# Kernel tuning notes

Hardware: AMD Instinct MI355X
Metric: run time of the kernel (lower is better)

The kernel has to match this reference:

```python
import jax, jax.numpy as jnp
import numpy as np

N, D, B = 8192, 512, 64
EPS = 1e-5


def _layernorm(x, w, b):
    mu = jnp.mean(x, axis=-1, keepdims=True)
    var = jnp.mean(jnp.square(x - mu), axis=-1, keepdims=True)
    return (x - mu) * jax.lax.rsqrt(var + EPS) * w + b


def setup_inputs() -> dict:
    key = jax.random.key(0)
    ks = jax.random.split(key, 10)
    s = 0.02
    return {
        "x_mole": jax.random.normal(ks[0], (N, D), jnp.float32),
        "x_conf": jax.random.normal(ks[1], (N, D), jnp.float32),
        "W1": jax.random.normal(ks[2], (D, D), jnp.float32) * s,   # attention_1 (no bias)
        "W2": jax.random.normal(ks[3], (D, D), jnp.float32) * s,   # attention_2 (no bias)
        "phi1_w": jnp.ones((D,), jnp.float32),
        "phi1_b": jnp.zeros((D,), jnp.float32),
        "phi2_w": jnp.ones((D,), jnp.float32),
        "phi2_b": jnp.zeros((D,), jnp.float32),
        "rho_w1": jax.random.normal(ks[4], (D, D), jnp.float32) * s,
        "rho_b1": jnp.zeros((D,), jnp.float32),
        "rho_w2": jax.random.normal(ks[5], (D, D), jnp.float32) * s,
        "rho_b2": jnp.zeros((D,), jnp.float32),
        "rho_ln_w": jnp.ones((D,), jnp.float32),
        "rho_ln_b": jnp.zeros((D,), jnp.float32),
        "batch": jnp.sort(jax.random.randint(ks[6], (N,), 0, B, jnp.int64)),
    }


def reference(x_mole, x_conf, W1, W2, phi1_w, phi1_b, phi2_w, phi2_b,
              rho_w1, rho_b1, rho_w2, rho_b2, rho_ln_w, rho_ln_b, batch):
    # projections of LayerNormed inputs (torch Linear: y = x @ W^T)
    q = _layernorm(x_mole, phi1_w, phi1_b) @ W1.T          # [N, D]
    k = _layernorm(x_conf, phi2_w, phi2_b) @ W2.T          # [N, D]
    dot = q @ k.T                                          # [N, N]

    # block-diagonal batch-equality mask and hand-rolled masked softmax
    mask = (batch[:, None] == batch[None, :]).astype(dot.dtype)  # [N, N]
    max_values = jnp.max(dot * mask, axis=1, keepdims=True)
    masked = (dot - max_values) * mask
    e = jnp.exp(masked)
    attn = e / jnp.sum(e * mask, axis=1, keepdims=True)
    attn = attn * mask                                     # [N, N]

    x_weighted = attn @ x_conf                             # [N, D]

    # rho MLP: Linear -> SiLU -> Linear -> SiLU -> LayerNorm
    h = jax.nn.silu(x_weighted @ rho_w1.T + rho_b1)
    h = jax.nn.silu(h @ rho_w2.T + rho_b2)
    x_encoded = _layernorm(h, rho_ln_w, rho_ln_b)
    return x_encoded, attn
```

## Files before the change

kernel.cpp:

```cpp
#include <hip/hip_runtime.h>

namespace {

constexpr int N = 8192;
constexpr int D = 512;
constexpr int NBATCH = 64;
constexpr int SEGMAX = 256;
constexpr int XCW = NBATCH * SEGMAX;
constexpr size_t MB = 1u << 20;

using s16x8 = __attribute__((ext_vector_type(8))) short;
using f32x4 = __attribute__((ext_vector_type(4))) float;

__device__ inline short f2bf(float f) {
  unsigned u = __float_as_uint(f);
  u += 0x7fffu + ((u >> 16) & 1u);
  return (short)(u >> 16);
}
__device__ inline float bf2f(short h) {
  return __uint_as_float(((unsigned)(unsigned short)h) << 16);
}
__device__ inline void split2(float f, short& hi, short& lo) {
  hi = f2bf(f);
  lo = f2bf(f - bf2f(hi));
}

__device__ inline f32x4 mfma16(s16x8 a, s16x8 b, f32x4 c) {
  return __builtin_amdgcn_mfma_f32_16x16x32_bf16(a, b, c, 0, 0, 0);
}

__device__ inline void gl16(const short* g, short* l) {
  __builtin_amdgcn_global_load_lds((const __attribute__((address_space(1))) void*)g,
                                   (__attribute__((address_space(3))) void*)l, 16, 0, 0);
}

template <int Nn>
__device__ inline void vmw() {
  asm volatile("s_waitcnt vmcnt(%0)" ::"i"(Nn) : "memory");
}

__device__ inline void ln_row(const float* __restrict__ x, const float* __restrict__ w,
                              const float* __restrict__ bsrc, int row, int lane,
                              float o[8]) {
  const float* xr = x + (size_t)row * D + lane * 8;
  f32x4 v0 = *(const f32x4*)xr;
  f32x4 v1 = *(const f32x4*)(xr + 4);
  float s = 0.f, sq = 0.f;
#pragma unroll
  for (int j = 0; j < 4; j++) {
    s += v0[j] + v1[j];
    sq += v0[j] * v0[j] + v1[j] * v1[j];
  }
#pragma unroll
  for (int off = 32; off >= 1; off >>= 1) {
    s += __shfl_xor(s, off);
    sq += __shfl_xor(sq, off);
  }
  float mu = s * (1.f / D);
  float var = sq * (1.f / D) - mu * mu;
  float rs = rsqrtf(var + 1e-5f);
  const float* wp = w + lane * 8;
  const float* bp = bsrc + lane * 8;
  f32x4 w0 = *(const f32x4*)wp, w1 = *(const f32x4*)(wp + 4);
  f32x4 b0 = *(const f32x4*)bp, b1 = *(const f32x4*)(bp + 4);
#pragma unroll
  for (int j = 0; j < 4; j++) {
    o[j] = (v0[j] - mu) * rs * w0[j] + b0[j];
    o[j + 4] = (v1[j] - mu) * rs * w1[j] + b1[j];
  }
}

__global__ __launch_bounds__(256) void prep_kernel(
    const float* __restrict__ x_mole, const float* __restrict__ phi1_w,
    const float* __restrict__ phi1_b, short* __restrict__ xm_hi, short* __restrict__ xm_lo,
    const float* __restrict__ x_conf, const float* __restrict__ phi2_w,
    const float* __restrict__ phi2_b, short* __restrict__ xc_hi, short* __restrict__ xc_lo,
    const float* __restrict__ W1, const float* __restrict__ W2,
    const float* __restrict__ rho_w1, const float* __restrict__ rho_w2,
    short* __restrict__ w1h, short* __restrict__ w1l,
    short* __restrict__ w2h, short* __restrict__ w2l,
    short* __restrict__ r1h, short* __restrict__ r1l,
    short* __restrict__ r2h, short* __restrict__ r2l,
    const int* __restrict__ batch, int* __restrict__ seg, int* __restrict__ colmap) {
  int bid = blockIdx.x;
  int tid = threadIdx.x;
  if (bid < 4096) {
    int inst = bid >> 11;
    int rowblk = bid & 2047;
    const float* x = inst ? x_conf : x_mole;
    const float* w = inst ? phi2_w : phi1_w;
    const float* b = inst ? phi2_b : phi1_b;
    short* oh = inst ? xc_hi : xm_hi;
    short* ol = inst ? xc_lo : xm_lo;
    int row = rowblk * 4 + (tid >> 6);
    int lane = tid & 63;
    float o[8];
    ln_row(x, w, b, row, lane, o);
    s16x8 hi, lo;
#pragma unroll
    for (int j = 0; j < 8; j++) {
      short h, l;
      split2(o[j], h, l);
      hi[j] = h; lo[j] = l;
    }
    *(s16x8*)(oh + (size_t)row * D + lane * 8) = hi;
    *(s16x8*)(ol + (size_t)row * D + lane * 8) = lo;
  } else if (bid < 4608) {
    int idx = bid - 4096;
    int mat = idx >> 7;
    const float* s = (mat == 0) ? W1 : (mat == 1) ? W2 : (mat == 2) ? rho_w1 : rho_w2;
    short* h = (mat == 0) ? w1h : (mat == 1) ? w2h : (mat == 2) ? r1h : r2h;
    short* l = (mat == 0) ? w1l : (mat == 1) ? w2l : (mat == 2) ? r1l : r2l;
    int i = (idx & 127) * 256 + tid;
    f32x4 a = *(const f32x4*)(s + (size_t)i * 8);
    f32x4 b = *(const f32x4*)(s + (size_t)i * 8 + 4);
    s16x8 oh, ol;
#pragma unroll
    for (int j = 0; j < 4; j++) {
      short hh, ll;
      split2(a[j], hh, ll); oh[j] = hh; ol[j] = ll;
      split2(b[j], hh, ll); oh[j + 4] = hh; ol[j + 4] = ll;
    }
    *(s16x8*)(h + (size_t)i * 8) = oh;
    *(s16x8*)(l + (size_t)i * 8) = ol;
  } else {
    int stride = (batch[N - 1] == 0) ? 2 : 1;
    if (tid <= NBATCH) {
      int lo = 0, hi = N;
      while (lo < hi) {
        int mid = (lo + hi) >> 1;
        if (batch[mid * stride] < tid) lo = mid + 1; else hi = mid;
      }
      seg[tid] = lo;
    }
    __syncthreads();
    for (int r = tid; r < N; r += 256) {
      int bb = batch[r * stride];
      colmap[r] = bb * SEGMAX + (r - seg[bb]);
    }
  }
}

__global__ __launch_bounds__(256) void ln_f32(const float* __restrict__ x,
                                              const float* __restrict__ w,
                                              const float* __restrict__ bsrc,
                                              float* __restrict__ out) {
  int row = blockIdx.x * 4 + (threadIdx.x >> 6);
  int lane = threadIdx.x & 63;
  float o[8];
  ln_row(x, w, bsrc, row, lane, o);
  f32x4 o0, o1;
#pragma unroll
  for (int j = 0; j < 4; j++) { o0[j] = o[j]; o1[j] = o[j + 4]; }
  float* op = out + (size_t)row * D + lane * 8;
  *(f32x4*)op = o0;
  *(f32x4*)(op + 4) = o1;
}

__global__ __launch_bounds__(256) void transpose_xc(const float* __restrict__ xc,
                                                    const int* __restrict__ colmap,
                                                    short* __restrict__ xcT) {
  __shared__ float tile[32][33];
  int tx = threadIdx.x & 31, ty = threadIdx.x >> 5;
  int r0 = blockIdx.x * 32, c0 = blockIdx.y * 32;
#pragma unroll
  for (int p = 0; p < 4; p++)
    tile[ty + p * 8][tx] = xc[(size_t)(r0 + ty + p * 8) * D + c0 + tx];
  __syncthreads();
  int cp = colmap[r0 + tx];
#pragma unroll
  for (int p = 0; p < 4; p++) {
    int d = c0 + ty + p * 8;
    xcT[(size_t)d * XCW + cp] = f2bf(tile[tx][ty + p * 8]);
  }
}

template <int SPLITA, int EPI>
__device__ void gemm_core(const short* __restrict__ Ahi, const short* __restrict__ Alo,
                          const short* __restrict__ Bhi, const short* __restrict__ Blo,
                          const float* __restrict__ bias, void* __restrict__ C0,
                          void* __restrict__ C1, short* lds, int bx, int by) {
  constexpr int ASZ = 64 * 32;
  constexpr int BSZ = 128 * 32;
  constexpr int AH = 0;
  constexpr int AL = ASZ;
  constexpr int BH = SPLITA ? 2 * ASZ : ASZ;
  constexpr int BL = BH + BSZ;
  constexpr int STEP = BL + BSZ;

  int tid = threadIdx.x;
  int w = tid >> 6, l = tid & 63, lr = l & 15, kg = l >> 4;
  int wm = w >> 1, wn = w & 1;
  int m_base = by * 64;
  int n_base = bx * 128;

  int srow = tid >> 2;
  int gch = (tid & 3) ^ ((tid >> 3) & 3);
  const short* a_h = Ahi + (size_t)(m_base + srow) * D + gch * 8;
  const short* a_l = SPLITA ? (Alo + (size_t)(m_base + srow) * D + gch * 8) : nullptr;
  const short* b_h = Bhi + (size_t)(n_base + srow) * D + gch * 8;
  const short* b_l = Blo + (size_t)(n_base + srow) * D + gch * 8;

  int aoff[2], boff[4];
#pragma unroll
  for (int fo = 0; fo < 2; fo++) {
    int row = wm * 32 + fo * 16 + lr;
    aoff[fo] = row * 32 + ((kg ^ ((row >> 1) & 3)) << 3);
  }
#pragma unroll
  for (int fo = 0; fo < 4; fo++) {
    int row = wn * 64 + fo * 16 + lr;
    boff[fo] = row * 32 + ((kg ^ ((row >> 1) & 3)) << 3);
  }

  f32x4 acc[2][4] = {};

  auto STAGE = [&](int c, int ko) {
    short* base = lds + c * STEP;
    gl16(a_h + ko, base + AH + w * 512);
    if (SPLITA) gl16(a_l + ko, base + AL + w * 512);
    gl16(b_h + ko, base + BH + w * 512);
    gl16(b_h + (size_t)64 * D + ko, base + BH + 2048 + w * 512);
    gl16(b_l + ko, base + BL + w * 512);
    gl16(b_l + (size_t)64 * D + ko, base + BL + 2048 + w * 512);
  };
  constexpr int LPS = SPLITA ? 6 : 5;

  STAGE(0, 0);
  STAGE(1, 32);
#pragma unroll
  for (int s = 0; s < 16; ++s) {
    const int cur = s & 1;
    if (s < 15) vmw<LPS>(); else vmw<0>();
    __builtin_amdgcn_s_barrier();
    __builtin_amdgcn_sched_barrier(0);
    const short* base = lds + cur * STEP;
    s16x8 av[2], alv[2], bv[4], blv[4];
#pragma unroll
    for (int i = 0; i < 2; i++) {
      av[i] = *(const s16x8*)(base + AH + aoff[i]);
      if (SPLITA) alv[i] = *(const s16x8*)(base + AL + aoff[i]);
    }
#pragma unroll
    for (int j = 0; j < 4; j++) {
      bv[j] = *(const s16x8*)(base + BH + boff[j]);
      blv[j] = *(const s16x8*)(base + BL + boff[j]);
    }
#pragma unroll
    for (int i = 0; i < 2; i++)
#pragma unroll
      for (int j = 0; j < 4; j++) {
        if (SPLITA)
          acc[i][j] = mfma16(av[i], bv[j],
                             mfma16(av[i], blv[j], mfma16(alv[i], bv[j], acc[i][j])));
        else
          acc[i][j] = mfma16(av[i], bv[j], mfma16(av[i], blv[j], acc[i][j]));
      }
    __builtin_amdgcn_sched_barrier(0);
    __builtin_amdgcn_s_barrier();
    __builtin_amdgcn_sched_barrier(0);
    if (s + 2 < 16) STAGE(cur, (s + 2) * 32);
  }

#pragma unroll
  for (int i = 0; i < 2; i++)
#pragma unroll
    for (int j = 0; j < 4; j++) {
      int col = n_base + wn * 64 + j * 16 + lr;
      float bv2 = (EPI >= 1) ? bias[col] : 0.f;
#pragma unroll
      for (int r = 0; r < 4; r++) {
        int rowg = m_base + wm * 32 + i * 16 + kg * 4 + r;
        float v = acc[i][j][r];
        if (EPI >= 1) { v += bv2; v = v / (1.f + __expf(-v)); }
        if (EPI == 0) {
          short h, lo2;
          split2(v, h, lo2);
          ((short*)C0)[(size_t)rowg * D + col] = h;
          ((short*)C1)[(size_t)rowg * D + col] = lo2;
        } else if (EPI == 1) {
          ((short*)C0)[(size_t)rowg * D + col] = f2bf(v);
        } else {
          ((float*)C0)[(size_t)rowg * D + col] = v;
        }
      }
    }
}

__global__ __launch_bounds__(256) void gemm_qk(
    const short* __restrict__ A0h, const short* __restrict__ A0l,
    const short* __restrict__ B0h, const short* __restrict__ B0l,
    short* __restrict__ C0h, short* __restrict__ C0l,
    const short* __restrict__ A1h, const short* __restrict__ A1l,
    const short* __restrict__ B1h, const short* __restrict__ B1l,
    short* __restrict__ C1h, short* __restrict__ C1l) {
  __shared__ short lds[2 * (2 * 64 * 32 + 2 * 128 * 32)];
  int z = blockIdx.z;
  int o = blockIdx.y * 4 + blockIdx.x;
  int xcd = o & 7, slot = o >> 3;
  int by = xcd * 16 + (slot >> 2);
  int bx = slot & 3;
  if (z == 0)
    gemm_core<1, 0>(A0h, A0l, B0h, B0l, nullptr, C0h, C0l, lds, bx, by);
  else
    gemm_core<1, 0>(A1h, A1l, B1h, B1l, nullptr, C1h, C1l, lds, bx, by);
}

template <int EPI>
__global__ __launch_bounds__(256) void gemm_rho(const short* __restrict__ Ahi,
                                                const short* __restrict__ Bhi,
                                                const short* __restrict__ Blo,
                                                const float* __restrict__ bias,
                                                void* __restrict__ C0) {
  __shared__ short lds[2 * (64 * 32 + 2 * 128 * 32)];
  int o = blockIdx.y * 4 + blockIdx.x;
  int xcd = o & 7, slot = o >> 3;
  int by = xcd * 16 + (slot >> 2);
  int bx = slot & 3;
  gemm_core<0, EPI>(Ahi, nullptr, Bhi, Blo, bias, C0, nullptr, lds, bx, by);
}

__global__ __launch_bounds__(256) void attn_kernel(const short* __restrict__ qh,
                                                   const short* __restrict__ ql,
                                                   const short* __restrict__ kh,
                                                   const short* __restrict__ kl,
                                                   const short* __restrict__ xcT,
                                                   const int* __restrict__ seg,
                                                   float* __restrict__ attn_out,
                                                   short* __restrict__ xw) {
  __shared__ float Ss[32][260];
  __shared__ short Ph[32][256];
  int b = blockIdx.y;
  int s0 = seg[b];
  int nb = seg[b + 1] - s0;
  int r0 = blockIdx.x * 32;
  if (r0 >= nb) return;
  int tid = threadIdx.x;
  int w = tid >> 6, l = tid & 63, lr = l & 15, kg = l >> 4;
  int row8 = tid >> 3, sub = tid & 7;
  bool rvalid = (r0 + row8) < nb;

  size_t q0 = (size_t)(s0 + r0 + lr) * D + kg * 8;
  size_t q1 = q0 + 16 * D;
  int ncf = (nb + 15) >> 4;
  for (int f = w; f < ncf; f += 4) {
    f32x4 a0 = {0, 0, 0, 0}, a1 = {0, 0, 0, 0};
    size_t kr = (size_t)(s0 + f * 16 + lr) * D + kg * 8;
    for (int k0 = 0; k0 < D; k0 += 32) {
      s16x8 kH = *(const s16x8*)(kh + kr + k0);
      s16x8 kL = *(const s16x8*)(kl + kr + k0);
      s16x8 qH0 = *(const s16x8*)(qh + q0 + k0);
      s16x8 qH1 = *(const s16x8*)(qh + q1 + k0);
      s16x8 qL0 = *(const s16x8*)(ql + q0 + k0);
      s16x8 qL1 = *(const s16x8*)(ql + q1 + k0);
      a0 = mfma16(qH0, kH, mfma16(qH0, kL, mfma16(qL0, kH, a0)));
      a1 = mfma16(qH1, kH, mfma16(qH1, kL, mfma16(qL1, kH, a1)));
    }
#pragma unroll
    for (int r = 0; r < 4; r++) {
      Ss[kg * 4 + r][f * 16 + lr] = a0[r];
      Ss[16 + kg * 4 + r][f * 16 + lr] = a1[r];
    }
  }
  __syncthreads();

  int nbp32 = (nb + 31) & ~31;
  if (rvalid) {
    float m = 0.f;
    for (int j = sub; j < nb; j += 8) m = fmaxf(m, Ss[row8][j]);
    m = fmaxf(m, __shfl_xor(m, 1));
    m = fmaxf(m, __shfl_xor(m, 2));
    m = fmaxf(m, __shfl_xor(m, 4));
    float sum = 0.f;
    for (int j = sub; j < nb; j += 8) {
      float e = __expf(Ss[row8][j] - m);
      Ss[row8][j] = e;
      sum += e;
    }
    sum += __shfl_xor(sum, 1);
    sum += __shfl_xor(sum, 2);
    sum += __shfl_xor(sum, 4);
    float inv = 1.f / sum;
    float* orow = attn_out + (size_t)(s0 + r0 + row8) * N + s0;
    for (int j = sub; j < nbp32; j += 8) {
      int sw = ((((j >> 3) ^ (row8 & 7)) << 3) | (j & 7));
      if (j < nb) {
        float a = Ss[row8][j] * inv;
        orow[j] = a;
        Ph[row8][sw] = f2bf(a);
      } else {
        Ph[row8][sw] = 0;
      }
    }
  }
  __syncthreads();

  for (int f2 = w * 8; f2 < w * 8 + 8; f2++) {
    f32x4 a0 = {0, 0, 0, 0}, a1 = {0, 0, 0, 0};
    const short* xrow = xcT + (size_t)(f2 * 16 + lr) * XCW + b * SEGMAX + kg * 8;
    for (int j0 = 0; j0 < nbp32; j0 += 32) {
      int ch = (j0 >> 3) + kg;
      int swo = ((ch ^ (lr & 7)) << 3);
      s16x8 pH0 = *(const s16x8*)&Ph[lr][swo];
      s16x8 pH1 = *(const s16x8*)&Ph[16 + lr][swo];
      s16x8 xv = *(const s16x8*)(xrow + j0);
      a0 = mfma16(pH0, xv, a0);
      a1 = mfma16(pH1, xv, a1);
    }
#pragma unroll
    for (int r = 0; r < 4; r++) {
      int rr0 = kg * 4 + r, rr1 = 16 + kg * 4 + r;
      if (r0 + rr0 < nb) xw[(size_t)(s0 + r0 + rr0) * D + f2 * 16 + lr] = f2bf(a0[r]);
      if (r0 + rr1 < nb) xw[(size_t)(s0 + r0 + rr1) * D + f2 * 16 + lr] = f2bf(a1[r]);
    }
  }
}

}

extern "C" void kernel_launch(void* const* d_in, const int* in_sizes, int n_in,
                              void* d_out, int out_size, void* d_ws, size_t ws_size,
                              hipStream_t stream) {
  (void)in_sizes; (void)n_in; (void)out_size; (void)ws_size;
  const float* x_mole = (const float*)d_in[0];
  const float* x_conf = (const float*)d_in[1];
  const float* W1 = (const float*)d_in[2];
  const float* W2 = (const float*)d_in[3];
  const float* phi1_w = (const float*)d_in[4];
  const float* phi1_b = (const float*)d_in[5];
  const float* phi2_w = (const float*)d_in[6];
  const float* phi2_b = (const float*)d_in[7];
  const float* rho_w1 = (const float*)d_in[8];
  const float* rho_b1 = (const float*)d_in[9];
  const float* rho_w2 = (const float*)d_in[10];
  const float* rho_b2 = (const float*)d_in[11];
  const float* rho_ln_w = (const float*)d_in[12];
  const float* rho_ln_b = (const float*)d_in[13];
  const int* batch = (const int*)d_in[14];

  float* out = (float*)d_out;
  float* attn_out = out + (size_t)N * D;

  char* w8 = (char*)d_ws;
  short* xm_hi = (short*)(w8 + 0 * MB);
  short* xm_lo = (short*)(w8 + 8 * MB);
  short* xc_hi = (short*)(w8 + 16 * MB);
  short* xc_lo = (short*)(w8 + 24 * MB);
  short* q_hi  = (short*)(w8 + 32 * MB);
  short* q_lo  = (short*)(w8 + 41 * MB);
  short* k_hi  = (short*)(w8 + 50 * MB);
  short* k_lo  = (short*)(w8 + 59 * MB);
  short* xcT   = (short*)(w8 + 68 * MB);
  short* w1h   = (short*)(w8 + 84 * MB);
  short* w1l   = (short*)(w8 + 84 * MB + 524288);
  short* w2h   = (short*)(w8 + 85 * MB);
  short* w2l   = (short*)(w8 + 85 * MB + 524288);
  short* r1h   = (short*)(w8 + 86 * MB);
  short* r1l   = (short*)(w8 + 86 * MB + 524288);
  short* r2h   = (short*)(w8 + 87 * MB);
  short* r2l   = (short*)(w8 + 87 * MB + 524288);
  int*   seg   = (int*)(w8 + 88 * MB);
  int*   colmap = (int*)(w8 + 88 * MB + 512);
  float* h2    = (float*)(w8 + 32 * MB);
  short* xw = xm_hi;
  short* h1 = xc_hi;

  hipMemsetAsync((void*)attn_out, 0, (size_t)N * N * sizeof(float), stream);

  prep_kernel<<<4609, 256, 0, stream>>>(
      x_mole, phi1_w, phi1_b, xm_hi, xm_lo,
      x_conf, phi2_w, phi2_b, xc_hi, xc_lo,
      W1, W2, rho_w1, rho_w2,
      w1h, w1l, w2h, w2l, r1h, r1l, r2h, r2l,
      batch, seg, colmap);
  transpose_xc<<<dim3(N / 32, D / 32), 256, 0, stream>>>(x_conf, colmap, xcT);
  gemm_qk<<<dim3(4, 128, 2), 256, 0, stream>>>(xm_hi, xm_lo, w1h, w1l, q_hi, q_lo,
                                               xc_hi, xc_lo, w2h, w2l, k_hi, k_lo);
  attn_kernel<<<dim3(SEGMAX / 32, NBATCH), 256, 0, stream>>>(q_hi, q_lo, k_hi, k_lo,
                                                             xcT, seg, attn_out, xw);
  gemm_rho<1><<<dim3(4, 128), 256, 0, stream>>>(xw, r1h, r1l, rho_b1, h1);
  gemm_rho<2><<<dim3(4, 128), 256, 0, stream>>>(h1, r2h, r2l, rho_b2, h2);
  ln_f32<<<N / 4, 256, 0, stream>>>(h2, rho_ln_w, rho_ln_b, out);
}
```

Measured before the change: 504.4 us.

## Fuse transpose into prep, widen QK GEMM tiles, drop split-bf16 in rho GEMMs

The x_conf transpose moves into prep_kernel, and each block now finds its column position with its own binary search instead of reading a precomputed colmap. That removes one kernel launch and the colmap pass. The QK projection GEMM now uses 256-wide N tiles, so there are fewer blocks and each A tile is reused more. The rho MLP GEMMs use plain bf16 weights instead of hi/lo split pairs, which halves B loads and MFMAs there but lowers the precision of those products.

```diff
diff --git a/kernel.cpp b/kernel.cpp
--- a/kernel.cpp
+++ b/kernel.cpp
@@ -79,9 +79,10 @@
     const float* __restrict__ rho_w1, const float* __restrict__ rho_w2,
     short* __restrict__ w1h, short* __restrict__ w1l,
     short* __restrict__ w2h, short* __restrict__ w2l,
-    short* __restrict__ r1h, short* __restrict__ r1l,
-    short* __restrict__ r2h, short* __restrict__ r2l,
-    const int* __restrict__ batch, int* __restrict__ seg, int* __restrict__ colmap) {
+    short* __restrict__ r1h, short* __restrict__ r2h,
+    short* __restrict__ xcT,
+    const int* __restrict__ batch, int* __restrict__ seg) {
+  __shared__ float tile[32][33];
   int bid = blockIdx.x;
   int tid = threadIdx.x;
   if (bid < 4096) {
@@ -109,20 +110,54 @@
     int idx = bid - 4096;
     int mat = idx >> 7;
     const float* s = (mat == 0) ? W1 : (mat == 1) ? W2 : (mat == 2) ? rho_w1 : rho_w2;
-    short* h = (mat == 0) ? w1h : (mat == 1) ? w2h : (mat == 2) ? r1h : r2h;
-    short* l = (mat == 0) ? w1l : (mat == 1) ? w2l : (mat == 2) ? r1l : r2l;
     int i = (idx & 127) * 256 + tid;
     f32x4 a = *(const f32x4*)(s + (size_t)i * 8);
     f32x4 b = *(const f32x4*)(s + (size_t)i * 8 + 4);
-    s16x8 oh, ol;
-#pragma unroll
-    for (int j = 0; j < 4; j++) {
-      short hh, ll;
-      split2(a[j], hh, ll); oh[j] = hh; ol[j] = ll;
-      split2(b[j], hh, ll); oh[j + 4] = hh; ol[j + 4] = ll;
-    }
-    *(s16x8*)(h + (size_t)i * 8) = oh;
-    *(s16x8*)(l + (size_t)i * 8) = ol;
+    if (mat < 2) {
+      short* h = (mat == 0) ? w1h : w2h;
+      short* l = (mat == 0) ? w1l : w2l;
+      s16x8 oh, ol;
+#pragma unroll
+      for (int j = 0; j < 4; j++) {
+        short hh, ll;
+        split2(a[j], hh, ll); oh[j] = hh; ol[j] = ll;
+        split2(b[j], hh, ll); oh[j + 4] = hh; ol[j + 4] = ll;
+      }
+      *(s16x8*)(h + (size_t)i * 8) = oh;
+      *(s16x8*)(l + (size_t)i * 8) = ol;
+    } else {
+      short* h = (mat == 2) ? r1h : r2h;
+      s16x8 oh;
+#pragma unroll
+      for (int j = 0; j < 4; j++) {
+        oh[j] = f2bf(a[j]);
+        oh[j + 4] = f2bf(b[j]);
+      }
+      *(s16x8*)(h + (size_t)i * 8) = oh;
+    }
+  } else if (bid < 8704) {
+    int idx = bid - 4608;
+    int r0 = (idx & 255) * 32;
+    int c0 = (idx >> 8) * 32;
+    int tx = tid & 31, ty = tid >> 5;
+#pragma unroll
+    for (int p = 0; p < 4; p++)
+      tile[ty + p * 8][tx] = x_conf[(size_t)(r0 + ty + p * 8) * D + c0 + tx];
+    __syncthreads();
+    int stride = (batch[N - 1] == 0) ? 2 : 1;
+    int r = r0 + tx;
+    int bb = batch[r * stride];
+    int lo = 0, hi = N;
+    while (lo < hi) {
+      int mid = (lo + hi) >> 1;
+      if (batch[mid * stride] < bb) lo = mid + 1; else hi = mid;
+    }
+    int cp = bb * SEGMAX + (r - lo);
+#pragma unroll
+    for (int p = 0; p < 4; p++) {
+      int d = c0 + ty + p * 8;
+      xcT[(size_t)d * XCW + cp] = f2bf(tile[tx][ty + p * 8]);
+    }
   } else {
     int stride = (batch[N - 1] == 0) ? 2 : 1;
     if (tid <= NBATCH) {
@@ -132,11 +167,6 @@
         if (batch[mid * stride] < tid) lo = mid + 1; else hi = mid;
       }
       seg[tid] = lo;
-    }
-    __syncthreads();
-    for (int r = tid; r < N; r += 256) {
-      int bb = batch[r * stride];
-      colmap[r] = bb * SEGMAX + (r - seg[bb]);
     }
   }
 }
@@ -157,74 +187,59 @@
   *(f32x4*)(op + 4) = o1;
 }
 
-__global__ __launch_bounds__(256) void transpose_xc(const float* __restrict__ xc,
-                                                    const int* __restrict__ colmap,
-                                                    short* __restrict__ xcT) {
-  __shared__ float tile[32][33];
-  int tx = threadIdx.x & 31, ty = threadIdx.x >> 5;
-  int r0 = blockIdx.x * 32, c0 = blockIdx.y * 32;
-#pragma unroll
-  for (int p = 0; p < 4; p++)
-    tile[ty + p * 8][tx] = xc[(size_t)(r0 + ty + p * 8) * D + c0 + tx];
-  __syncthreads();
-  int cp = colmap[r0 + tx];
-#pragma unroll
-  for (int p = 0; p < 4; p++) {
-    int d = c0 + ty + p * 8;
-    xcT[(size_t)d * XCW + cp] = f2bf(tile[tx][ty + p * 8]);
-  }
-}
-
-template <int SPLITA, int EPI>
+template <int BN, int SPLITA, int SPLITB, int EPI>
 __device__ void gemm_core(const short* __restrict__ Ahi, const short* __restrict__ Alo,
                           const short* __restrict__ Bhi, const short* __restrict__ Blo,
                           const float* __restrict__ bias, void* __restrict__ C0,
                           void* __restrict__ C1, short* lds, int bx, int by) {
   constexpr int ASZ = 64 * 32;
-  constexpr int BSZ = 128 * 32;
+  constexpr int BSZ = BN * 32;
   constexpr int AH = 0;
   constexpr int AL = ASZ;
-  constexpr int BH = SPLITA ? 2 * ASZ : ASZ;
+  constexpr int BH = ASZ * (1 + SPLITA);
   constexpr int BL = BH + BSZ;
-  constexpr int STEP = BL + BSZ;
+  constexpr int STEP = BH + BSZ * (1 + SPLITB);
+  constexpr int NB64 = BN / 64;
+  constexpr int NF = BN / 32;
 
   int tid = threadIdx.x;
   int w = tid >> 6, l = tid & 63, lr = l & 15, kg = l >> 4;
   int wm = w >> 1, wn = w & 1;
   int m_base = by * 64;
-  int n_base = bx * 128;
+  int n_base = bx * BN;
 
   int srow = tid >> 2;
   int gch = (tid & 3) ^ ((tid >> 3) & 3);
   const short* a_h = Ahi + (size_t)(m_base + srow) * D + gch * 8;
   const short* a_l = SPLITA ? (Alo + (size_t)(m_base + srow) * D + gch * 8) : nullptr;
   const short* b_h = Bhi + (size_t)(n_base + srow) * D + gch * 8;
-  const short* b_l = Blo + (size_t)(n_base + srow) * D + gch * 8;
-
-  int aoff[2], boff[4];
+  const short* b_l = SPLITB ? (Blo + (size_t)(n_base + srow) * D + gch * 8) : nullptr;
+
+  int aoff[2], boff[NF];
 #pragma unroll
   for (int fo = 0; fo < 2; fo++) {
     int row = wm * 32 + fo * 16 + lr;
     aoff[fo] = row * 32 + ((kg ^ ((row >> 1) & 3)) << 3);
   }
 #pragma unroll
-  for (int fo = 0; fo < 4; fo++) {
-    int row = wn * 64 + fo * 16 + lr;
+  for (int fo = 0; fo < NF; fo++) {
+    int row = wn * (BN / 2) + fo * 16 + lr;
     boff[fo] = row * 32 + ((kg ^ ((row >> 1) & 3)) << 3);
   }
 
-  f32x4 acc[2][4] = {};
+  f32x4 acc[2][NF] = {};
 
   auto STAGE = [&](int c, int ko) {
     short* base = lds + c * STEP;
     gl16(a_h + ko, base + AH + w * 512);
     if (SPLITA) gl16(a_l + ko, base + AL + w * 512);
-    gl16(b_h + ko, base + BH + w * 512);
-    gl16(b_h + (size_t)64 * D + ko, base + BH + 2048 + w * 512);
-    gl16(b_l + ko, base + BL + w * 512);
-    gl16(b_l + (size_t)64 * D + ko, base + BL + 2048 + w * 512);
+#pragma unroll
+    for (int cb = 0; cb < NB64; cb++) {
+      gl16(b_h + (size_t)(cb * 64) * D + ko, base + BH + cb * 2048 + w * 512);
+      if (SPLITB) gl16(b_l + (size_t)(cb * 64) * D + ko, base + BL + cb * 2048 + w * 512);
+    }
   };
-  constexpr int LPS = SPLITA ? 6 : 5;
+  constexpr int LPS = 1 + SPLITA + NB64 * (1 + SPLITB);
 
   STAGE(0, 0);
   STAGE(1, 32);
@@ -235,26 +250,28 @@
     __builtin_amdgcn_s_barrier();
     __builtin_amdgcn_sched_barrier(0);
     const short* base = lds + cur * STEP;
-    s16x8 av[2], alv[2], bv[4], blv[4];
+    s16x8 av[2], alv[2], bv[NF], blv[NF];
 #pragma unroll
     for (int i = 0; i < 2; i++) {
       av[i] = *(const s16x8*)(base + AH + aoff[i]);
       if (SPLITA) alv[i] = *(const s16x8*)(base + AL + aoff[i]);
     }
 #pragma unroll
-    for (int j = 0; j < 4; j++) {
+    for (int j = 0; j < NF; j++) {
       bv[j] = *(const s16x8*)(base + BH + boff[j]);
-      blv[j] = *(const s16x8*)(base + BL + boff[j]);
+      if (SPLITB) blv[j] = *(const s16x8*)(base + BL + boff[j]);
     }
 #pragma unroll
     for (int i = 0; i < 2; i++)
 #pragma unroll
-      for (int j = 0; j < 4; j++) {
-        if (SPLITA)
+      for (int j = 0; j < NF; j++) {
+        if (SPLITA && SPLITB)
           acc[i][j] = mfma16(av[i], bv[j],
                              mfma16(av[i], blv[j], mfma16(alv[i], bv[j], acc[i][j])));
+        else if (SPLITB)
+          acc[i][j] = mfma16(av[i], bv[j], mfma16(av[i], blv[j], acc[i][j]));
         else
-          acc[i][j] = mfma16(av[i], bv[j], mfma16(av[i], blv[j], acc[i][j]));
+          acc[i][j] = mfma16(av[i], bv[j], acc[i][j]);
       }
     __builtin_amdgcn_sched_barrier(0);
     __builtin_amdgcn_s_barrier();
@@ -265,8 +282,8 @@
 #pragma unroll
   for (int i = 0; i < 2; i++)
 #pragma unroll
-    for (int j = 0; j < 4; j++) {
-      int col = n_base + wn * 64 + j * 16 + lr;
+    for (int j = 0; j < NF; j++) {
+      int col = n_base + wn * (BN / 2) + j * 16 + lr;
       float bv2 = (EPI >= 1) ? bias[col] : 0.f;
 #pragma unroll
       for (int r = 0; r < 4; r++) {
@@ -294,30 +311,28 @@
     const short* __restrict__ A1h, const short* __restrict__ A1l,
     const short* __restrict__ B1h, const short* __restrict__ B1l,
     short* __restrict__ C1h, short* __restrict__ C1l) {
-  __shared__ short lds[2 * (2 * 64 * 32 + 2 * 128 * 32)];
-  int z = blockIdx.z;
+  __shared__ short lds[2 * (2 * 64 * 32 + 2 * 256 * 32)];
+  int o = blockIdx.y * 2 + blockIdx.x;
+  int xcd = o & 7, slot = o >> 3;
+  int by = xcd * 16 + (slot >> 1);
+  int bx = slot & 1;
+  if (blockIdx.z == 0)
+    gemm_core<256, 1, 1, 0>(A0h, A0l, B0h, B0l, nullptr, C0h, C0l, lds, bx, by);
+  else
+    gemm_core<256, 1, 1, 0>(A1h, A1l, B1h, B1l, nullptr, C1h, C1l, lds, bx, by);
+}
+
+template <int EPI>
+__global__ __launch_bounds__(256) void gemm_rho(const short* __restrict__ Ahi,
+                                                const short* __restrict__ Bhi,
+                                                const float* __restrict__ bias,
+                                                void* __restrict__ C0) {
+  __shared__ short lds[2 * (64 * 32 + 128 * 32)];
   int o = blockIdx.y * 4 + blockIdx.x;
   int xcd = o & 7, slot = o >> 3;
   int by = xcd * 16 + (slot >> 2);
   int bx = slot & 3;
-  if (z == 0)
-    gemm_core<1, 0>(A0h, A0l, B0h, B0l, nullptr, C0h, C0l, lds, bx, by);
-  else
-    gemm_core<1, 0>(A1h, A1l, B1h, B1l, nullptr, C1h, C1l, lds, bx, by);
-}
-
-template <int EPI>
-__global__ __launch_bounds__(256) void gemm_rho(const short* __restrict__ Ahi,
-                                                const short* __restrict__ Bhi,
-                                                const short* __restrict__ Blo,
-                                                const float* __restrict__ bias,
-                                                void* __restrict__ C0) {
-  __shared__ short lds[2 * (64 * 32 + 2 * 128 * 32)];
-  int o = blockIdx.y * 4 + blockIdx.x;
-  int xcd = o & 7, slot = o >> 3;
-  int by = xcd * 16 + (slot >> 2);
-  int bx = slot & 3;
-  gemm_core<0, EPI>(Ahi, nullptr, Bhi, Blo, bias, C0, nullptr, lds, bx, by);
+  gemm_core<128, 0, 0, EPI>(Ahi, nullptr, Bhi, nullptr, bias, C0, nullptr, lds, bx, by);
 }
 
 __global__ __launch_bounds__(256) void attn_kernel(const short* __restrict__ qh,
@@ -456,29 +471,25 @@
   short* w2h   = (short*)(w8 + 85 * MB);
   short* w2l   = (short*)(w8 + 85 * MB + 524288);
   short* r1h   = (short*)(w8 + 86 * MB);
-  short* r1l   = (short*)(w8 + 86 * MB + 524288);
   short* r2h   = (short*)(w8 + 87 * MB);
-  short* r2l   = (short*)(w8 + 87 * MB + 524288);
   int*   seg   = (int*)(w8 + 88 * MB);
-  int*   colmap = (int*)(w8 + 88 * MB + 512);
   float* h2    = (float*)(w8 + 32 * MB);
   short* xw = xm_hi;
   short* h1 = xc_hi;
 
   hipMemsetAsync((void*)attn_out, 0, (size_t)N * N * sizeof(float), stream);
 
-  prep_kernel<<<4609, 256, 0, stream>>>(
+  prep_kernel<<<8705, 256, 0, stream>>>(
       x_mole, phi1_w, phi1_b, xm_hi, xm_lo,
       x_conf, phi2_w, phi2_b, xc_hi, xc_lo,
       W1, W2, rho_w1, rho_w2,
-      w1h, w1l, w2h, w2l, r1h, r1l, r2h, r2l,
-      batch, seg, colmap);
-  transpose_xc<<<dim3(N / 32, D / 32), 256, 0, stream>>>(x_conf, colmap, xcT);
-  gemm_qk<<<dim3(4, 128, 2), 256, 0, stream>>>(xm_hi, xm_lo, w1h, w1l, q_hi, q_lo,
+      w1h, w1l, w2h, w2l, r1h, r2h,
+      xcT, batch, seg);
+  gemm_qk<<<dim3(2, 128, 2), 256, 0, stream>>>(xm_hi, xm_lo, w1h, w1l, q_hi, q_lo,
                                                xc_hi, xc_lo, w2h, w2l, k_hi, k_lo);
   attn_kernel<<<dim3(SEGMAX / 32, NBATCH), 256, 0, stream>>>(q_hi, q_lo, k_hi, k_lo,
                                                              xcT, seg, attn_out, xw);
-  gemm_rho<1><<<dim3(4, 128), 256, 0, stream>>>(xw, r1h, r1l, rho_b1, h1);
-  gemm_rho<2><<<dim3(4, 128), 256, 0, stream>>>(h1, r2h, r2l, rho_b2, h2);
+  gemm_rho<1><<<dim3(4, 128), 256, 0, stream>>>(xw, r1h, rho_b1, h1);
+  gemm_rho<2><<<dim3(4, 128), 256, 0, stream>>>(h1, r2h, rho_b2, h2);
   ln_f32<<<N / 4, 256, 0, stream>>>(h2, rho_ln_w, rho_ln_b, out);
 }
```

Result: faster. 488.5 us, median of 2 (-3.1%).
